# Kernel tuning notes

Measured on AMD Instinct MI355X. Metric: run time of the kernel, lower is better.

## Reference

```python
import jax, jax.numpy as jnp
import numpy as np

B, N, D = 4, 64, 64          # batch, n_nodes, state_dim
FN, FE, INTER, T = 32, 16, 128, 3


def setup_inputs() -> dict:
    key = jax.random.key(0)
    ks = jax.random.split(key, 12)
    conn = (jax.random.uniform(ks[0], (B, N * N, 1)) < 0.3).astype(jnp.float32)
    feat = jax.random.uniform(ks[1], (B, N * N, FE - 1))
    edges = jnp.concatenate([conn, feat], axis=-1)
    nodes = jax.random.normal(ks[2], (B, N, FN))
    adjacency = jnp.zeros((B, N * N, 1))  # unused (adjacency=False)
    s = lambda i, sh, fan: jax.random.normal(ks[i], sh) * (1.0 / np.sqrt(fan))
    return dict(
        edges=edges, nodes=nodes, adjacency=adjacency,
        W_en=s(3, (FN, D), FN), b_en=jnp.zeros(D),
        W_agg=s(4, (FE, D * D), FE), b_agg=jnp.zeros(D * D),
        W_ih=s(5, (3 * D, D), D), W_hh=s(6, (3 * D, D), D),
        b_ih=jnp.zeros(3 * D), b_hh=jnp.zeros(3 * D),
        W_r1=s(7, (2 * D + FE, INTER), 2 * D + FE), b_r1=jnp.zeros(INTER),
        W_r2=s(8, (INTER, INTER), INTER), b_r2=jnp.zeros(INTER),
        W_r3=s(9, (INTER, 1), INTER), b_r3=jnp.zeros(1),
    )


def _gru_cell(x, h, W_ih, W_hh, b_ih, b_hh):
    # PyTorch nn.GRU cell: gates ordered (r, z, n)
    gi = x @ W_ih.T + b_ih
    gh = h @ W_hh.T + b_hh
    ir, iz, inn = jnp.split(gi, 3, axis=-1)
    hr, hz, hn = jnp.split(gh, 3, axis=-1)
    r = jax.nn.sigmoid(ir + hr)
    z = jax.nn.sigmoid(iz + hz)
    n = jnp.tanh(inn + r * hn)
    return (1.0 - z) * n + z * h


def reference(edges, nodes, adjacency, W_en, b_en, W_agg, b_agg,
              W_ih, W_hh, b_ih, b_hh, W_r1, b_r1, W_r2, b_r2, W_r3, b_r3):
    # mask: torch.where(x==0, x, ones) on first edge feature -> {0,1}
    mask = jnp.where(edges[..., :1] == 0, 0.0, 1.0)  # [B, N*N, 1]
    h = jax.nn.relu(nodes @ W_en + b_en)  # [B, N, D]
    for _ in range(T):
        # per-edge dynamic weight matrices A: [B, N*N, D, D]
        A = jax.nn.relu(edges @ W_agg + b_agg).reshape(B, N * N, D, D)
        node_j = jnp.tile(h, (1, N, 1))  # [B, N*N, D]
        msgs = jnp.einsum('beij,bej->bei', A, node_j) * mask  # [B, N*N, D]
        agg = msgs.reshape(B, N, N, D).sum(2)  # [B, N, D]
        hf = h.reshape(-1, D)
        af = agg.reshape(-1, D)
        # GRU over length-2 sequence [old_state, agg_messages], h0 = 0; take last
        h1 = _gru_cell(hf, jnp.zeros_like(hf), W_ih, W_hh, b_ih, b_hh)
        h2 = _gru_cell(af, h1, W_ih, W_hh, b_ih, b_hh)
        h = h2.reshape(B, N, D)
    # Readout over all node pairs
    state_i = jnp.repeat(h, N, axis=1)      # [B, N*N, D] (node i repeated)
    state_j = jnp.tile(h, (1, N, 1))        # [B, N*N, D]
    cat = jnp.concatenate([state_i, edges, state_j], axis=-1)
    a1 = jax.nn.relu(cat @ W_r1 + b_r1)
    a2 = jax.nn.relu(a1 @ W_r2 + b_r2)
    return a2 @ W_r3 + b_r3  # [B, N*N, 1]
```

## Files before the change

### kernel.cpp

```cpp
#include <hip/hip_runtime.h>

typedef float float4v __attribute__((ext_vector_type(4)));

__device__ __forceinline__ float sigm(float x) { return 1.0f / (1.0f + __expf(-x)); }

#define HS_LD 68

__global__ __launch_bounds__(256) void k_pre(
    const float* __restrict__ nodes, const float* __restrict__ W_en,
    const float* __restrict__ b_en, const float* __restrict__ edges,
    const float* __restrict__ W_r1,
    float* __restrict__ h0, int* __restrict__ rowcnt, int* __restrict__ rowlist,
    float* __restrict__ epack, float* __restrict__ EW)
{
    __shared__ float eS[256];
    int t = threadIdx.x;
    if (blockIdx.x < 64) {
        int idx = blockIdx.x * 256 + t;
        int d = idx & 63, bn = idx >> 6;
        const float* np_ = nodes + bn * 32;
        float acc = b_en[d];
#pragma unroll
        for (int k = 0; k < 32; ++k)
            acc = fmaf(np_[k], W_en[k * 64 + d], acc);
        h0[idx] = fmaxf(acc, 0.f);
    } else if (blockIdx.x < 128) {
        int row = (blockIdx.x - 64) * 4 + (t >> 6);
        int lane = t & 63;
        const float* ep = edges + ((size_t)row * 64 + lane) * 16;
        bool act = ep[0] != 0.f;
        unsigned long long m = __ballot(act);
        if (lane == 0) rowcnt[row] = __popcll(m);
        if (act) {
            int pos = __popcll(m & ((1ull << lane) - 1ull));
            rowlist[row * 64 + pos] = lane;
            float* dst = epack + (size_t)row * 1024 + pos * 16;
#pragma unroll
            for (int u = 0; u < 4; ++u)
                *(float4v*)(dst + u * 4) = *(const float4v*)(ep + u * 4);
        }
    } else {
        int base = (blockIdx.x - 128) * 16;
        eS[t] = edges[(size_t)base * 16 + t];
        __syncthreads();
        int pp = t >> 7, d = t & 127;
#pragma unroll
        for (int pi = 0; pi < 8; ++pi) {
            int pl = pp * 8 + pi;
            float acc = 0.f;
#pragma unroll
            for (int k = 0; k < 16; ++k)
                acc = fmaf(eS[pl * 16 + k], W_r1[(64 + k) * 128 + d], acc);
            EW[(size_t)(base + pl) * 128 + d] = acc;
        }
    }
}

__global__ __launch_bounds__(1024, 1) void k_ig(
    const float* __restrict__ epack, const float* __restrict__ W_agg,
    const float* __restrict__ b_agg,
    const float* __restrict__ W_ih, const float* __restrict__ W_hh,
    const float* __restrict__ b_ih, const float* __restrict__ b_hh,
    const int* __restrict__ rowcnt, const int* __restrict__ rowlist,
    const float* __restrict__ h_cur, float* __restrict__ h_next,
    const float* __restrict__ W_r1, const float* __restrict__ b_r1,
    float* __restrict__ Ha, float* __restrict__ Hc, int emit)
{
    __shared__ float hs[64 * HS_LD];
    __shared__ float xtra[768];

    int t = threadIdx.x;
    int row = blockIdx.x;
    int ri = row & 63;
    int b = row >> 6;

    {
        int n = t >> 4, col = (t & 15) * 4;
        *(float4v*)(hs + n * HS_LD + col) =
            *(const float4v*)(h_cur + ((b << 6) + n) * 64 + col);
    }

    int dim = t >> 4, c4 = t & 15, lane = t & 63;

    float4v w[16];
    {
        const float* wp = W_agg + dim * 64 + c4 * 4;
#pragma unroll
        for (int k = 0; k < 16; ++k)
            w[k] = *(const float4v*)(wp + k * 4096);
    }
    float4v bias = *(const float4v*)(b_agg + dim * 64 + c4 * 4);

    int rl = rowlist[row * 64 + lane];
    int nE = rowcnt[row];
    __syncthreads();

    const float* eb = epack + (size_t)row * 1024;
    float rsum = 0.f;
    float4v n0 = {0,0,0,0}, n1 = n0, n2 = n0, n3 = n0;
    if (nE > 0) {
        n0 = *(const float4v*)(eb);      n1 = *(const float4v*)(eb + 4);
        n2 = *(const float4v*)(eb + 8);  n3 = *(const float4v*)(eb + 12);
    }
    for (int idx = 0; idx < nE; ++idx) {
        float4v e0 = n0, e1 = n1, e2 = n2, e3 = n3;
        if (idx + 1 < nE) {
            const float* ep = eb + (idx + 1) * 16;
            n0 = *(const float4v*)(ep);      n1 = *(const float4v*)(ep + 4);
            n2 = *(const float4v*)(ep + 8);  n3 = *(const float4v*)(ep + 12);
        }
        int ej = __shfl(rl, idx, 64);
        float4v a = bias;
#pragma unroll
        for (int k = 0; k < 4; ++k) {
#pragma unroll
            for (int u = 0; u < 4; ++u) a[u] = fmaf(e0[k], w[k][u], a[u]);
        }
#pragma unroll
        for (int k = 0; k < 4; ++k) {
#pragma unroll
            for (int u = 0; u < 4; ++u) a[u] = fmaf(e1[k], w[4 + k][u], a[u]);
        }
#pragma unroll
        for (int k = 0; k < 4; ++k) {
#pragma unroll
            for (int u = 0; u < 4; ++u) a[u] = fmaf(e2[k], w[8 + k][u], a[u]);
        }
#pragma unroll
        for (int k = 0; k < 4; ++k) {
#pragma unroll
            for (int u = 0; u < 4; ++u) a[u] = fmaf(e3[k], w[12 + k][u], a[u]);
        }
        float4v hv = *(const float4v*)(hs + ej * HS_LD + c4 * 4);
#pragma unroll
        for (int u = 0; u < 4; ++u)
            rsum = fmaf(fmaxf(a[u], 0.f), hv[u], rsum);
    }
#pragma unroll
    for (int m = 1; m < 16; m <<= 1) rsum += __shfl_xor(rsum, m, 64);
    float* aggS = xtra;
    if (c4 == 0) aggS[dim] = rsum;
    __syncthreads();

    float* g1  = xtra + 64;
    float* h1S = xtra + 256;
    float* g2i = xtra + 320;
    float* g2h = xtra + 512;
    float* hnS = xtra + 704;
    const float* hrow = hs + ri * HS_LD;

    if (t < 192) {
        float g = b_ih[t];
        const float* wr = W_ih + t * 64;
#pragma unroll
        for (int k = 0; k < 64; ++k) g = fmaf(hrow[k], wr[k], g);
        g1[t] = g;
    }
    __syncthreads();
    if (t < 64) {
        float r1 = sigm(g1[t] + b_hh[t]);
        float z1 = sigm(g1[64 + t] + b_hh[64 + t]);
        float nn1 = tanhf(g1[128 + t] + r1 * b_hh[128 + t]);
        h1S[t] = (1.f - z1) * nn1;
    }
    __syncthreads();
    if (t < 192) {
        float gi = b_ih[t];
        float gh = b_hh[t];
        const float* wri = W_ih + t * 64;
        const float* wrh = W_hh + t * 64;
#pragma unroll
        for (int k = 0; k < 64; ++k) {
            gi = fmaf(aggS[k], wri[k], gi);
            gh = fmaf(h1S[k], wrh[k], gh);
        }
        g2i[t] = gi; g2h[t] = gh;
    }
    __syncthreads();
    if (t < 64) {
        float r = sigm(g2i[t] + g2h[t]);
        float z = sigm(g2i[64 + t] + g2h[64 + t]);
        float nn = tanhf(g2i[128 + t] + r * g2h[128 + t]);
        float hn = (1.f - z) * nn + z * h1S[t];
        h_next[row * 64 + t] = hn;
        hnS[t] = hn;
    }
    __syncthreads();
    if (emit && t < 256) {
        int m = t >> 7, d = t & 127;
        const float* wbase = W_r1 + (m ? 80 * 128 : 0) + d;
        float acc = m ? 0.f : b_r1[d];
#pragma unroll
        for (int k = 0; k < 64; ++k)
            acc = fmaf(hnS[k], wbase[k * 128], acc);
        if (m == 0) Ha[row * 128 + d] = acc;
        else        Hc[row * 128 + d] = acc;
    }
}

__global__ __launch_bounds__(256) void k_read(
    const float* __restrict__ EW, const float* __restrict__ Ha,
    const float* __restrict__ Hc,
    const float* __restrict__ W_r2, const float* __restrict__ b_r2,
    const float* __restrict__ W_r3, const float* __restrict__ b_r3,
    float* __restrict__ out)
{
    __shared__ float HaS[128];
    __shared__ float A1[32 * 128];
    int t = threadIdx.x;
    int unit = blockIdx.x;
    int row = unit >> 1, qp = unit & 1;
    int b = row >> 6;

    const float* src = Hc + (size_t)((b << 6) + qp * 32) * 128;
#pragma unroll
    for (int r = 0; r < 4; ++r) {
        int off = (r * 256 + t) * 4;
        *(float4v*)(A1 + off) = *(const float4v*)(src + off);
    }
    if (t < 32)
        *(float4v*)(HaS + t * 4) = *(const float4v*)(Ha + (size_t)row * 128 + t * 4);
    __syncthreads();

    const float* EWrow = EW + (size_t)(row * 64 + qp * 32) * 128;
#pragma unroll
    for (int r = 0; r < 4; ++r) {
        int off = (r * 256 + t) * 4;
        int dd = off & 127;
        float4v hc = *(const float4v*)(A1 + off);
        float4v ha = *(const float4v*)(HaS + dd);
        float4v ew = *(const float4v*)(EWrow + off);
        float4v a;
#pragma unroll
        for (int u = 0; u < 4; ++u) a[u] = fmaxf(hc[u] + ha[u] + ew[u], 0.f);
        *(float4v*)(A1 + off) = a;
    }
    __syncthreads();

    int td = t & 31, pg = t >> 5;
    float4v bb2 = *(const float4v*)(b_r2 + td * 4);
    float4v acc0 = bb2, acc1 = bb2, acc2 = bb2, acc3 = bb2;
    for (int k4 = 0; k4 < 32; ++k4) {
        float4v wA = *(const float4v*)(W_r2 + (k4 * 4 + 0) * 128 + td * 4);
        float4v wB = *(const float4v*)(W_r2 + (k4 * 4 + 1) * 128 + td * 4);
        float4v wC = *(const float4v*)(W_r2 + (k4 * 4 + 2) * 128 + td * 4);
        float4v wD = *(const float4v*)(W_r2 + (k4 * 4 + 3) * 128 + td * 4);
        float4v a0 = *(const float4v*)(A1 + (pg * 4 + 0) * 128 + k4 * 4);
        float4v a1 = *(const float4v*)(A1 + (pg * 4 + 1) * 128 + k4 * 4);
        float4v a2 = *(const float4v*)(A1 + (pg * 4 + 2) * 128 + k4 * 4);
        float4v a3 = *(const float4v*)(A1 + (pg * 4 + 3) * 128 + k4 * 4);
#pragma unroll
        for (int u = 0; u < 4; ++u) {
            acc0[u] = fmaf(a0[0], wA[u], acc0[u]);
            acc0[u] = fmaf(a0[1], wB[u], acc0[u]);
            acc0[u] = fmaf(a0[2], wC[u], acc0[u]);
            acc0[u] = fmaf(a0[3], wD[u], acc0[u]);
            acc1[u] = fmaf(a1[0], wA[u], acc1[u]);
            acc1[u] = fmaf(a1[1], wB[u], acc1[u]);
            acc1[u] = fmaf(a1[2], wC[u], acc1[u]);
            acc1[u] = fmaf(a1[3], wD[u], acc1[u]);
            acc2[u] = fmaf(a2[0], wA[u], acc2[u]);
            acc2[u] = fmaf(a2[1], wB[u], acc2[u]);
            acc2[u] = fmaf(a2[2], wC[u], acc2[u]);
            acc2[u] = fmaf(a2[3], wD[u], acc2[u]);
            acc3[u] = fmaf(a3[0], wA[u], acc3[u]);
            acc3[u] = fmaf(a3[1], wB[u], acc3[u]);
            acc3[u] = fmaf(a3[2], wC[u], acc3[u]);
            acc3[u] = fmaf(a3[3], wD[u], acc3[u]);
        }
    }

    float4v w3v = *(const float4v*)(W_r3 + td * 4);
    float b3 = b_r3[0];
    float p0 = fmaxf(acc0[0], 0.f) * w3v[0] + fmaxf(acc0[1], 0.f) * w3v[1]
             + fmaxf(acc0[2], 0.f) * w3v[2] + fmaxf(acc0[3], 0.f) * w3v[3];
    float p1 = fmaxf(acc1[0], 0.f) * w3v[0] + fmaxf(acc1[1], 0.f) * w3v[1]
             + fmaxf(acc1[2], 0.f) * w3v[2] + fmaxf(acc1[3], 0.f) * w3v[3];
    float p2 = fmaxf(acc2[0], 0.f) * w3v[0] + fmaxf(acc2[1], 0.f) * w3v[1]
             + fmaxf(acc2[2], 0.f) * w3v[2] + fmaxf(acc2[3], 0.f) * w3v[3];
    float p3 = fmaxf(acc3[0], 0.f) * w3v[0] + fmaxf(acc3[1], 0.f) * w3v[1]
             + fmaxf(acc3[2], 0.f) * w3v[2] + fmaxf(acc3[3], 0.f) * w3v[3];
#pragma unroll
    for (int m = 1; m < 32; m <<= 1) {
        p0 += __shfl_xor(p0, m, 64);
        p1 += __shfl_xor(p1, m, 64);
        p2 += __shfl_xor(p2, m, 64);
        p3 += __shfl_xor(p3, m, 64);
    }
    if (td == 0) {
        int obase = row * 64 + qp * 32 + pg * 4;
        out[obase + 0] = p0 + b3;
        out[obase + 1] = p1 + b3;
        out[obase + 2] = p2 + b3;
        out[obase + 3] = p3 + b3;
    }
}

extern "C" void kernel_launch(void* const* d_in, const int* in_sizes, int n_in,
                              void* d_out, int out_size, void* d_ws, size_t ws_size,
                              hipStream_t stream)
{
    const float* edges = (const float*)d_in[0];
    const float* nodes = (const float*)d_in[1];
    const float* W_en  = (const float*)d_in[3];
    const float* b_en  = (const float*)d_in[4];
    const float* W_agg = (const float*)d_in[5];
    const float* b_agg = (const float*)d_in[6];
    const float* W_ih  = (const float*)d_in[7];
    const float* W_hh  = (const float*)d_in[8];
    const float* b_ih  = (const float*)d_in[9];
    const float* b_hh  = (const float*)d_in[10];
    const float* W_r1  = (const float*)d_in[11];
    const float* b_r1  = (const float*)d_in[12];
    const float* W_r2  = (const float*)d_in[13];
    const float* b_r2  = (const float*)d_in[14];
    const float* W_r3  = (const float*)d_in[15];
    const float* b_r3  = (const float*)d_in[16];

    int*   rowcnt  = (int*)d_ws;
    int*   rowlist = rowcnt + 256;
    float* hA      = (float*)(rowlist + 16384);
    float* hB      = hA + 16384;
    float* Ha      = hB + 16384;
    float* Hc      = Ha + 256 * 128;
    float* epack   = Hc + 256 * 128;
    float* EW      = epack + 256 * 1024;
    float* out     = (float*)d_out;

    k_pre<<<1152, 256, 0, stream>>>(nodes, W_en, b_en, edges, W_r1,
                                    hA, rowcnt, rowlist, epack, EW);
    k_ig<<<256, 1024, 0, stream>>>(epack, W_agg, b_agg, W_ih, W_hh, b_ih, b_hh,
                                   rowcnt, rowlist, hA, hB, W_r1, b_r1, Ha, Hc, 0);
    k_ig<<<256, 1024, 0, stream>>>(epack, W_agg, b_agg, W_ih, W_hh, b_ih, b_hh,
                                   rowcnt, rowlist, hB, hA, W_r1, b_r1, Ha, Hc, 0);
    k_ig<<<256, 1024, 0, stream>>>(epack, W_agg, b_agg, W_ih, W_hh, b_ih, b_hh,
                                   rowcnt, rowlist, hA, hB, W_r1, b_r1, Ha, Hc, 1);
    k_read<<<512, 256, 0, stream>>>(EW, Ha, Hc, W_r2, b_r2, W_r3, b_r3, out);
}
```

Measured before the change: 95.63 us.

## Fold preprocessing kernel into iteration and readout kernels, drop packed buffers

Removes the separate k_pre launch. The first GRU iteration now computes the node encoding itself. Each iteration block compacts its own row's active edges into shared memory instead of reading a pre-packed global buffer. The readout kernel computes the edge contribution to W_r1 on the fly instead of reading a precomputed EW array. This saves one launch and several global round-trips, at the cost of redundant node encoding per block in iteration 0 and repeated edge compaction in every iteration. Also relaxes launch_bounds minimum blocks.

```diff
diff --git a/kernel.cpp b/kernel.cpp
--- a/kernel.cpp
+++ b/kernel.cpp
@@ -6,67 +6,20 @@
 
 #define HS_LD 68
 
-__global__ __launch_bounds__(256) void k_pre(
-    const float* __restrict__ nodes, const float* __restrict__ W_en,
-    const float* __restrict__ b_en, const float* __restrict__ edges,
-    const float* __restrict__ W_r1,
-    float* __restrict__ h0, int* __restrict__ rowcnt, int* __restrict__ rowlist,
-    float* __restrict__ epack, float* __restrict__ EW)
-{
-    __shared__ float eS[256];
-    int t = threadIdx.x;
-    if (blockIdx.x < 64) {
-        int idx = blockIdx.x * 256 + t;
-        int d = idx & 63, bn = idx >> 6;
-        const float* np_ = nodes + bn * 32;
-        float acc = b_en[d];
-#pragma unroll
-        for (int k = 0; k < 32; ++k)
-            acc = fmaf(np_[k], W_en[k * 64 + d], acc);
-        h0[idx] = fmaxf(acc, 0.f);
-    } else if (blockIdx.x < 128) {
-        int row = (blockIdx.x - 64) * 4 + (t >> 6);
-        int lane = t & 63;
-        const float* ep = edges + ((size_t)row * 64 + lane) * 16;
-        bool act = ep[0] != 0.f;
-        unsigned long long m = __ballot(act);
-        if (lane == 0) rowcnt[row] = __popcll(m);
-        if (act) {
-            int pos = __popcll(m & ((1ull << lane) - 1ull));
-            rowlist[row * 64 + pos] = lane;
-            float* dst = epack + (size_t)row * 1024 + pos * 16;
-#pragma unroll
-            for (int u = 0; u < 4; ++u)
-                *(float4v*)(dst + u * 4) = *(const float4v*)(ep + u * 4);
-        }
-    } else {
-        int base = (blockIdx.x - 128) * 16;
-        eS[t] = edges[(size_t)base * 16 + t];
-        __syncthreads();
-        int pp = t >> 7, d = t & 127;
-#pragma unroll
-        for (int pi = 0; pi < 8; ++pi) {
-            int pl = pp * 8 + pi;
-            float acc = 0.f;
-#pragma unroll
-            for (int k = 0; k < 16; ++k)
-                acc = fmaf(eS[pl * 16 + k], W_r1[(64 + k) * 128 + d], acc);
-            EW[(size_t)(base + pl) * 128 + d] = acc;
-        }
-    }
-}
-
-__global__ __launch_bounds__(1024, 1) void k_ig(
-    const float* __restrict__ epack, const float* __restrict__ W_agg,
-    const float* __restrict__ b_agg,
+__global__ __launch_bounds__(1024) void k_it(
+    const float* __restrict__ edges, const float* __restrict__ nodes,
+    const float* __restrict__ W_en, const float* __restrict__ b_en,
+    const float* __restrict__ W_agg, const float* __restrict__ b_agg,
     const float* __restrict__ W_ih, const float* __restrict__ W_hh,
     const float* __restrict__ b_ih, const float* __restrict__ b_hh,
-    const int* __restrict__ rowcnt, const int* __restrict__ rowlist,
     const float* __restrict__ h_cur, float* __restrict__ h_next,
     const float* __restrict__ W_r1, const float* __restrict__ b_r1,
-    float* __restrict__ Ha, float* __restrict__ Hc, int emit)
+    float* __restrict__ Ha, float* __restrict__ Hc, int it0, int emit)
 {
     __shared__ float hs[64 * HS_LD];
+    __shared__ float eL[64 * 16];
+    __shared__ int   jn[64];
+    __shared__ int   nES;
     __shared__ float xtra[768];
 
     int t = threadIdx.x;
@@ -74,14 +27,40 @@
     int ri = row & 63;
     int b = row >> 6;
 
-    {
+    if (it0) {
+#pragma unroll
+        for (int q = 0; q < 4; ++q) {
+            int idx = q * 1024 + t;
+            int n = idx >> 6, d = idx & 63;
+            const float* np_ = nodes + ((b << 6) + n) * 32;
+            float acc = b_en[d];
+#pragma unroll
+            for (int k = 0; k < 32; ++k)
+                acc = fmaf(np_[k], W_en[k * 64 + d], acc);
+            hs[n * HS_LD + d] = fmaxf(acc, 0.f);
+        }
+    } else {
         int n = t >> 4, col = (t & 15) * 4;
         *(float4v*)(hs + n * HS_LD + col) =
             *(const float4v*)(h_cur + ((b << 6) + n) * 64 + col);
     }
 
-    int dim = t >> 4, c4 = t & 15, lane = t & 63;
-
+    if (t < 64) {
+        const float* ep = edges + ((size_t)row * 64 + t) * 16;
+        float f0 = ep[0];
+        unsigned long long m = __ballot(f0 != 0.f);
+        if (t == 0) nES = __popcll(m);
+        if (f0 != 0.f) {
+            int pos = __popcll(m & ((1ull << t) - 1ull));
+            jn[pos] = t;
+            float* dst = eL + pos * 16;
+#pragma unroll
+            for (int u = 0; u < 4; ++u)
+                *(float4v*)(dst + u * 4) = *(const float4v*)(ep + u * 4);
+        }
+    }
+
+    int dim = t >> 4, c4 = t & 15;
     float4v w[16];
     {
         const float* wp = W_agg + dim * 64 + c4 * 4;
@@ -91,25 +70,17 @@
     }
     float4v bias = *(const float4v*)(b_agg + dim * 64 + c4 * 4);
 
-    int rl = rowlist[row * 64 + lane];
-    int nE = rowcnt[row];
-    __syncthreads();
-
-    const float* eb = epack + (size_t)row * 1024;
+    __syncthreads();
+    int nE = nES;
+
     float rsum = 0.f;
-    float4v n0 = {0,0,0,0}, n1 = n0, n2 = n0, n3 = n0;
-    if (nE > 0) {
-        n0 = *(const float4v*)(eb);      n1 = *(const float4v*)(eb + 4);
-        n2 = *(const float4v*)(eb + 8);  n3 = *(const float4v*)(eb + 12);
-    }
-    for (int idx = 0; idx < nE; ++idx) {
-        float4v e0 = n0, e1 = n1, e2 = n2, e3 = n3;
-        if (idx + 1 < nE) {
-            const float* ep = eb + (idx + 1) * 16;
-            n0 = *(const float4v*)(ep);      n1 = *(const float4v*)(ep + 4);
-            n2 = *(const float4v*)(ep + 8);  n3 = *(const float4v*)(ep + 12);
-        }
-        int ej = __shfl(rl, idx, 64);
+    for (int s = 0; s < nE; ++s) {
+        const float* eP = eL + s * 16;
+        float4v e0 = *(const float4v*)(eP);
+        float4v e1 = *(const float4v*)(eP + 4);
+        float4v e2 = *(const float4v*)(eP + 8);
+        float4v e3 = *(const float4v*)(eP + 12);
+        int ej = jn[s];
         float4v a = bias;
 #pragma unroll
         for (int k = 0; k < 4; ++k) {
@@ -199,13 +170,15 @@
 }
 
 __global__ __launch_bounds__(256) void k_read(
-    const float* __restrict__ EW, const float* __restrict__ Ha,
-    const float* __restrict__ Hc,
+    const float* __restrict__ edges,
+    const float* __restrict__ Ha, const float* __restrict__ Hc,
+    const float* __restrict__ W_r1,
     const float* __restrict__ W_r2, const float* __restrict__ b_r2,
     const float* __restrict__ W_r3, const float* __restrict__ b_r3,
     float* __restrict__ out)
 {
     __shared__ float HaS[128];
+    __shared__ float eS[32 * 16];
     __shared__ float A1[32 * 128];
     int t = threadIdx.x;
     int unit = blockIdx.x;
@@ -220,24 +193,42 @@
     }
     if (t < 32)
         *(float4v*)(HaS + t * 4) = *(const float4v*)(Ha + (size_t)row * 128 + t * 4);
-    __syncthreads();
-
-    const float* EWrow = EW + (size_t)(row * 64 + qp * 32) * 128;
-#pragma unroll
-    for (int r = 0; r < 4; ++r) {
-        int off = (r * 256 + t) * 4;
-        int dd = off & 127;
-        float4v hc = *(const float4v*)(A1 + off);
-        float4v ha = *(const float4v*)(HaS + dd);
-        float4v ew = *(const float4v*)(EWrow + off);
+    if (t < 128)
+        *(float4v*)(eS + t * 4) =
+            *(const float4v*)(edges + ((size_t)row * 64 + qp * 32) * 16 + t * 4);
+    __syncthreads();
+
+    int td = t & 31, pg = t >> 5;
+
+    float4v ew0 = {0,0,0,0}, ew1 = ew0, ew2 = ew0, ew3 = ew0;
+#pragma unroll
+    for (int k = 0; k < 16; ++k) {
+        float4v wk = *(const float4v*)(W_r1 + (64 + k) * 128 + td * 4);
+        float e0 = eS[(pg * 4 + 0) * 16 + k];
+        float e1 = eS[(pg * 4 + 1) * 16 + k];
+        float e2 = eS[(pg * 4 + 2) * 16 + k];
+        float e3 = eS[(pg * 4 + 3) * 16 + k];
+#pragma unroll
+        for (int u = 0; u < 4; ++u) {
+            ew0[u] = fmaf(e0, wk[u], ew0[u]);
+            ew1[u] = fmaf(e1, wk[u], ew1[u]);
+            ew2[u] = fmaf(e2, wk[u], ew2[u]);
+            ew3[u] = fmaf(e3, wk[u], ew3[u]);
+        }
+    }
+    float4v ha = *(const float4v*)(HaS + td * 4);
+#pragma unroll
+    for (int pi = 0; pi < 4; ++pi) {
+        float4v ew = (pi == 0) ? ew0 : (pi == 1) ? ew1 : (pi == 2) ? ew2 : ew3;
+        float* slot = A1 + (pg * 4 + pi) * 128 + td * 4;
+        float4v hc = *(const float4v*)slot;
         float4v a;
 #pragma unroll
         for (int u = 0; u < 4; ++u) a[u] = fmaxf(hc[u] + ha[u] + ew[u], 0.f);
-        *(float4v*)(A1 + off) = a;
-    }
-    __syncthreads();
-
-    int td = t & 31, pg = t >> 5;
+        *(float4v*)slot = a;
+    }
+    __syncthreads();
+
     float4v bb2 = *(const float4v*)(b_r2 + td * 4);
     float4v acc0 = bb2, acc1 = bb2, acc2 = bb2, acc3 = bb2;
     for (int k4 = 0; k4 < 32; ++k4) {
@@ -317,23 +308,21 @@
     const float* W_r3  = (const float*)d_in[15];
     const float* b_r3  = (const float*)d_in[16];
 
-    int*   rowcnt  = (int*)d_ws;
-    int*   rowlist = rowcnt + 256;
-    float* hA      = (float*)(rowlist + 16384);
-    float* hB      = hA + 16384;
-    float* Ha      = hB + 16384;
-    float* Hc      = Ha + 256 * 128;
-    float* epack   = Hc + 256 * 128;
-    float* EW      = epack + 256 * 1024;
-    float* out     = (float*)d_out;
-
-    k_pre<<<1152, 256, 0, stream>>>(nodes, W_en, b_en, edges, W_r1,
-                                    hA, rowcnt, rowlist, epack, EW);
-    k_ig<<<256, 1024, 0, stream>>>(epack, W_agg, b_agg, W_ih, W_hh, b_ih, b_hh,
-                                   rowcnt, rowlist, hA, hB, W_r1, b_r1, Ha, Hc, 0);
-    k_ig<<<256, 1024, 0, stream>>>(epack, W_agg, b_agg, W_ih, W_hh, b_ih, b_hh,
-                                   rowcnt, rowlist, hB, hA, W_r1, b_r1, Ha, Hc, 0);
-    k_ig<<<256, 1024, 0, stream>>>(epack, W_agg, b_agg, W_ih, W_hh, b_ih, b_hh,
-                                   rowcnt, rowlist, hA, hB, W_r1, b_r1, Ha, Hc, 1);
-    k_read<<<512, 256, 0, stream>>>(EW, Ha, Hc, W_r2, b_r2, W_r3, b_r3, out);
+    float* hA = (float*)d_ws;
+    float* hB = hA + 16384;
+    float* Ha = hB + 16384;
+    float* Hc = Ha + 256 * 128;
+    float* out = (float*)d_out;
+
+    k_it<<<256, 1024, 0, stream>>>(edges, nodes, W_en, b_en, W_agg, b_agg,
+                                   W_ih, W_hh, b_ih, b_hh, hA, hA,
+                                   W_r1, b_r1, Ha, Hc, 1, 0);
+    k_it<<<256, 1024, 0, stream>>>(edges, nodes, W_en, b_en, W_agg, b_agg,
+                                   W_ih, W_hh, b_ih, b_hh, hA, hB,
+                                   W_r1, b_r1, Ha, Hc, 0, 0);
+    k_it<<<256, 1024, 0, stream>>>(edges, nodes, W_en, b_en, W_agg, b_agg,
+                                   W_ih, W_hh, b_ih, b_hh, hB, hA,
+                                   W_r1, b_r1, Ha, Hc, 0, 1);
+    k_read<<<512, 256, 0, stream>>>(edges, Ha, Hc, W_r1, W_r2, b_r2,
+                                    W_r3, b_r3, out);
 }
```

Measured after the change: 83.19 us. -13.0%, faster.
